# Kernel tuning notes

Hardware: AMD Instinct MI355X
Metric: run time of the kernel (lower is better)

The kernel has to match this reference:

```python
import jax, jax.numpy as jnp
import numpy as np
from jax import lax

STRIDE = 2
PADDING = 2
KERNEL = 5


def _conv_transpose3d(x, weight, bias):
    # weight: [C_in, C_out, kd, kh, kw] (PyTorch ConvTranspose3d layout)
    # Equivalent dense conv: flip kernel spatially, swap in/out channels,
    # lhs_dilation=stride, symmetric padding = dilation*(k-1) - padding.
    w_t = jnp.flip(weight, axis=(2, 3, 4)).transpose(1, 0, 2, 3, 4)  # [C_out, C_in, k,k,k]
    pad = KERNEL - 1 - PADDING  # = 2
    y = lax.conv_general_dilated(
        x, w_t,
        window_strides=(1, 1, 1),
        padding=[(pad, pad)] * 3,
        lhs_dilation=(STRIDE, STRIDE, STRIDE),
        dimension_numbers=("NCDHW", "OIDHW", "NCDHW"),
    )
    return y + bias[None, :, None, None, None]


def _maxpool3d(y, k):
    # PyTorch MaxPool3d(kernel=k) -> stride=k, no padding, floor mode == VALID
    win = (1, 1, k, k, k)
    return lax.reduce_window(y, -jnp.inf, lax.max, win, win, "VALID")


def setup_inputs() -> dict:
    key = jax.random.key(0)
    k1, k2, k3 = jax.random.split(key, 3)
    x = jax.random.normal(k1, (16, 32, 16, 32, 32), dtype=jnp.float32)
    weight = jax.random.normal(k2, (32, 64, 5, 5, 5), dtype=jnp.float32) * 0.05
    bias = jax.random.normal(k3, (64,), dtype=jnp.float32) * 0.05
    return {"x": x, "weight": weight, "bias": bias}


def reference(x, weight, bias):
    y = _conv_transpose3d(x, weight, bias)     # [16, 64, 31, 63, 63]
    y = _maxpool3d(y, 2)                       # [16, 64, 15, 31, 31]
    y = _maxpool3d(y, 3)                       # [16, 64, 5, 10, 10]
    return jnp.sum(y, axis=1, keepdims=True)   # [16, 1, 5, 10, 10]
```

## Files before the change

### kernel.cpp

```cpp
#include <hip/hip_runtime.h>
#include <hip/hip_bf16.h>
#include <math.h>

typedef short bf16x8 __attribute__((ext_vector_type(8)));
typedef float f32x4 __attribute__((ext_vector_type(4)));

constexpr int CIN = 32, COUT = 64, D = 16, H = 32, W = 32;

constexpr size_t WS_NEED = 884736u;

static __device__ const unsigned char IT_CODE[24] = {
    0, 8, 16, 3,
    1, 9, 17, 11, 19, 7,
    2, 10, 18, 5, 13, 21, 15,
    4, 12, 20, 6, 14, 22, 23};
static __device__ const unsigned char IT_START[5] = {0, 4, 10, 17, 24};
static __device__ const unsigned char EPI_START[10] = {0, 1, 3, 5, 6, 7, 9, 11, 12, 13};
static __device__ const unsigned char EPI_CNT[10]   = {1, 2, 2, 1, 1, 2, 2, 1, 1, 2};

__global__ void prep_w(const float* __restrict__ w, unsigned short* __restrict__ wtp) {
    int idx = blockIdx.x * 256 + threadIdx.x;
    int ci  = idx & 31;
    int co  = (idx >> 5) & 63;
    int tt  = idx >> 11;
    int t   = tt % 27, cls = tt / 27;
    int td = t / 9, th = (t / 3) % 3, tw = t % 3;
    int pd = (cls >> 2) & 1, ph = (cls >> 1) & 1, pw = cls & 1;
    int kd = pd + 2 * td, kh = ph + 2 * th, kw = pw + 2 * tw;
    float v = 0.f;
    if (kd < 5 && kh < 5 && kw < 5)
        v = w[(ci * COUT + co) * 125 + kd * 25 + kh * 5 + kw];
    __hip_bfloat16 b = __float2bfloat16(v);
    wtp[idx] = *reinterpret_cast<unsigned short*>(&b);
}

__device__ __forceinline__ int lpA(int wrow, int quad) {
    return wrow * 64 + ((quad ^ ((wrow >> 1) & 3)) << 4);
}

__global__ __launch_bounds__(256, 2) void main_k(
    const unsigned short* __restrict__ wtp, const float* __restrict__ x,
    const float* __restrict__ bias, float* __restrict__ out)
{
    __shared__ unsigned short Xs[25600];
    int bx = blockIdx.x;
    int h0 = bx % 10;
    int d0 = (bx / 10) % 5;
    int n  = bx / 50;
    int tid = threadIdx.x;

    int id0 = 3 * d0 - 1, ih0 = 3 * h0 - 1;
    for (int u = tid; u < 6400; u += 256) {
        int q  = u & 7;
        int ci = (u >> 3) & 31;
        int p  = u >> 8;
        int dd = p / 5, hl = p % 5;
        int id = id0 + dd, ih = ih0 + hl;
        float4 v = {0.f, 0.f, 0.f, 0.f};
        if (id >= 0 && ih >= 0)
            v = ((const float4*)(x + (((size_t)(n * CIN + ci) * D + id) * H + ih) * W))[q];
        unsigned short hj[4];
        {
            __hip_bfloat16 b0 = __float2bfloat16(v.x); hj[0] = *reinterpret_cast<unsigned short*>(&b0);
            __hip_bfloat16 b1 = __float2bfloat16(v.y); hj[1] = *reinterpret_cast<unsigned short*>(&b1);
            __hip_bfloat16 b2 = __float2bfloat16(v.z); hj[2] = *reinterpret_cast<unsigned short*>(&b2);
            __hip_bfloat16 b3 = __float2bfloat16(v.w); hj[3] = *reinterpret_cast<unsigned short*>(&b3);
        }
        int rowb = p * 1024;
        int cig = ci >> 3, cil = ci & 7;
#pragma unroll
        for (int j = 0; j < 4; ++j) {
            int ww = 4 * q + 1 + j;
            if (ww < 32)
                Xs[rowb + ww * 32 + ((cig ^ ((ww >> 1) & 3)) << 3) + cil] = hj[j];
        }
        if (q == 0)
            Xs[rowb + (cig << 3) + cil] = 0;
    }

    int lane = tid & 63, wv = tid >> 6;
    int l15 = lane & 15, quad = lane >> 4;
    int wv_s = __builtin_amdgcn_readfirstlane(wv);

    int laneB = l15 * 64 + quad * 16;
    int m1 = 16 + l15; if (m1 > 29) m1 = 29;
    int lp00 = lpA(l15 + 0, quad), lp01 = lpA(l15 + 1, quad), lp02 = lpA(l15 + 2, quad);
    int lp10 = lpA(m1 + 0, quad),  lp11 = lpA(m1 + 1, quad),  lp12 = lpA(m1 + 2, quad);

    f32x4 mx[2][4];
#pragma unroll
    for (int mt = 0; mt < 2; ++mt)
#pragma unroll
        for (int nt = 0; nt < 4; ++nt) mx[mt][nt] = (f32x4){-INFINITY, -INFINITY, -INFINITY, -INFINITY};

    __syncthreads();
    const char* xsb = (const char*)Xs;

    int it0 = IT_START[wv_s], it1 = IT_START[wv_s + 1];
#pragma unroll 1
    for (int ii = it0; ii < it1; ++ii) {
        int code  = __builtin_amdgcn_readfirstlane(IT_CODE[ii]);
        int cls   = code & 7;
        int alpha = code >> 3;
        int ntd = 3 - ((cls >> 2) & 1), nth = 3 - ((cls >> 1) & 1), ntw = 3 - (cls & 1);
        const char* tbb = (const char*)wtp + (size_t)cls * 27 * 4096 + laneB;
        const int T = ntd * nth * ntw;

        f32x4 acc[3][2][4];
#pragma unroll
        for (int b = 0; b < 3; ++b)
#pragma unroll
            for (int mt = 0; mt < 2; ++mt)
#pragma unroll
                for (int nt = 0; nt < 4; ++nt) acc[b][mt][nt] = (f32x4){0.f, 0.f, 0.f, 0.f};

        int ptd = 0, pth = 0, ptw = 0;
        auto adv = [&]() {
            ++ptw;
            if (ptw == ntw) { ptw = 0; ++pth; if (pth == nth) { pth = 0; ++ptd; } }
        };

        int Qb_e = ((alpha + 2) * 5 + 2) * 2048, ss_e = 2;
        bf16x8 bE0 = *(const bf16x8*)(tbb);
        bf16x8 bE1 = *(const bf16x8*)(tbb + 1024);
        bf16x8 bE2 = *(const bf16x8*)(tbb + 2048);
        bf16x8 bE3 = *(const bf16x8*)(tbb + 3072);
        adv();
        int Qb_o = ((alpha + 2 - ptd) * 5 + (2 - pth)) * 2048, ss_o = 2 - ptw;
        const char* bqo = tbb + (ptd * 9 + pth * 3 + ptw) * 4096;
        bf16x8 bO0 = *(const bf16x8*)(bqo);
        bf16x8 bO1 = *(const bf16x8*)(bqo + 1024);
        bf16x8 bO2 = *(const bf16x8*)(bqo + 2048);
        bf16x8 bO3 = *(const bf16x8*)(bqo + 3072);
        adv();

#pragma unroll 1
        for (int it = 0; it < T; it += 2) {
            {
                int lpa = ss_e == 0 ? lp00 : (ss_e == 1 ? lp01 : lp02);
                int lpb = ss_e == 0 ? lp10 : (ss_e == 1 ? lp11 : lp12);
#pragma unroll
                for (int beta = 0; beta < 3; ++beta) {
                    const char* rb = xsb + Qb_e + beta * 2048;
                    bf16x8 af0 = *(const bf16x8*)(rb + lpa);
                    bf16x8 af1 = *(const bf16x8*)(rb + lpb);
                    acc[beta][0][0] = __builtin_amdgcn_mfma_f32_16x16x32_bf16(af0, bE0, acc[beta][0][0], 0, 0, 0);
                    acc[beta][0][1] = __builtin_amdgcn_mfma_f32_16x16x32_bf16(af0, bE1, acc[beta][0][1], 0, 0, 0);
                    acc[beta][0][2] = __builtin_amdgcn_mfma_f32_16x16x32_bf16(af0, bE2, acc[beta][0][2], 0, 0, 0);
                    acc[beta][0][3] = __builtin_amdgcn_mfma_f32_16x16x32_bf16(af0, bE3, acc[beta][0][3], 0, 0, 0);
                    acc[beta][1][0] = __builtin_amdgcn_mfma_f32_16x16x32_bf16(af1, bE0, acc[beta][1][0], 0, 0, 0);
                    acc[beta][1][1] = __builtin_amdgcn_mfma_f32_16x16x32_bf16(af1, bE1, acc[beta][1][1], 0, 0, 0);
                    acc[beta][1][2] = __builtin_amdgcn_mfma_f32_16x16x32_bf16(af1, bE2, acc[beta][1][2], 0, 0, 0);
                    acc[beta][1][3] = __builtin_amdgcn_mfma_f32_16x16x32_bf16(af1, bE3, acc[beta][1][3], 0, 0, 0);
                }
            }
            if (it + 2 < T) {
                const char* bq = tbb + (ptd * 9 + pth * 3 + ptw) * 4096;
                Qb_e = ((alpha + 2 - ptd) * 5 + (2 - pth)) * 2048;
                ss_e = 2 - ptw;
                bE0 = *(const bf16x8*)(bq);
                bE1 = *(const bf16x8*)(bq + 1024);
                bE2 = *(const bf16x8*)(bq + 2048);
                bE3 = *(const bf16x8*)(bq + 3072);
                adv();
            }
            if (it + 1 < T) {
                {
                    int lpa = ss_o == 0 ? lp00 : (ss_o == 1 ? lp01 : lp02);
                    int lpb = ss_o == 0 ? lp10 : (ss_o == 1 ? lp11 : lp12);
#pragma unroll
                    for (int beta = 0; beta < 3; ++beta) {
                        const char* rb = xsb + Qb_o + beta * 2048;
                        bf16x8 af0 = *(const bf16x8*)(rb + lpa);
                        bf16x8 af1 = *(const bf16x8*)(rb + lpb);
                        acc[beta][0][0] = __builtin_amdgcn_mfma_f32_16x16x32_bf16(af0, bO0, acc[beta][0][0], 0, 0, 0);
                        acc[beta][0][1] = __builtin_amdgcn_mfma_f32_16x16x32_bf16(af0, bO1, acc[beta][0][1], 0, 0, 0);
                        acc[beta][0][2] = __builtin_amdgcn_mfma_f32_16x16x32_bf16(af0, bO2, acc[beta][0][2], 0, 0, 0);
                        acc[beta][0][3] = __builtin_amdgcn_mfma_f32_16x16x32_bf16(af0, bO3, acc[beta][0][3], 0, 0, 0);
                        acc[beta][1][0] = __builtin_amdgcn_mfma_f32_16x16x32_bf16(af1, bO0, acc[beta][1][0], 0, 0, 0);
                        acc[beta][1][1] = __builtin_amdgcn_mfma_f32_16x16x32_bf16(af1, bO1, acc[beta][1][1], 0, 0, 0);
                        acc[beta][1][2] = __builtin_amdgcn_mfma_f32_16x16x32_bf16(af1, bO2, acc[beta][1][2], 0, 0, 0);
                        acc[beta][1][3] = __builtin_amdgcn_mfma_f32_16x16x32_bf16(af1, bO3, acc[beta][1][3], 0, 0, 0);
                    }
                }
                if (it + 3 < T) {
                    const char* bq = tbb + (ptd * 9 + pth * 3 + ptw) * 4096;
                    Qb_o = ((alpha + 2 - ptd) * 5 + (2 - pth)) * 2048;
                    ss_o = 2 - ptw;
                    bO0 = *(const bf16x8*)(bq);
                    bO1 = *(const bf16x8*)(bq + 1024);
                    bO2 = *(const bf16x8*)(bq + 2048);
                    bO3 = *(const bf16x8*)(bq + 3072);
                    adv();
                }
            }
        }

#pragma unroll
        for (int mt = 0; mt < 2; ++mt)
#pragma unroll
            for (int nt = 0; nt < 4; ++nt)
#pragma unroll
                for (int r = 0; r < 4; ++r) {
                    float m = fmaxf(fmaxf(acc[0][mt][nt][r], acc[1][mt][nt][r]), acc[2][mt][nt][r]);
                    mx[mt][nt][r] = fmaxf(mx[mt][nt][r], m);
                }
    }

    __syncthreads();
    float* epi = (float*)Xs;
    int fsm0 = (0x3123 >> (quad * 4)) & 15;
    int fsm1 = (0x4312 >> (quad * 4)) & 15;
#pragma unroll
    for (int mt = 0; mt < 2; ++mt) {
        int fs = mt ? fsm1 : fsm0;
        int g  = mt * 4 + quad;
#pragma unroll
        for (int nt = 0; nt < 4; ++nt) {
            float a0 = mx[mt][nt][0], a1 = mx[mt][nt][1], a2 = mx[mt][nt][2], a3 = mx[mt][nt][3];
            float t01 = fmaxf(a0, a1), t012 = fmaxf(t01, a2), t0123 = fmaxf(t012, a3);
            float pA = fs == 1 ? a0 : (fs == 2 ? t01 : (fs == 3 ? t012 : t0123));
            float t23 = fmaxf(a2, a3), t123 = fmaxf(a1, t23);
            float pB = fs == 1 ? t123 : (fs == 2 ? t23 : (fs == 3 ? a3 : -INFINITY));
            epi[((wv * 8 + g) * 2 + 0) * 64 + nt * 16 + l15] = pA;
            epi[((wv * 8 + g) * 2 + 1) * 64 + nt * 16 + l15] = pB;
        }
    }
    __syncthreads();

    int elemBase = ((n * 5 + d0) * 10 + h0) * 10;
    float bco = bias[lane];
#pragma unroll 1
    for (int win = wv_s; win < 10; win += 4) {
        int st = EPI_START[win], cnt = EPI_CNT[win];
        float v = -INFINITY;
        for (int src = 0; src < 4; ++src)
            for (int e = st; e < st + cnt; ++e)
                v = fmaxf(v, epi[(src * 16 + e) * 64 + lane]);
        v += bco;
#pragma unroll
        for (int off = 32; off > 0; off >>= 1) v += __shfl_xor(v, off);
        if (lane == 0) out[elemBase + win] = v;
    }
}

__global__ __launch_bounds__(256) void fused_fallback(
    const float* __restrict__ x, const float* __restrict__ wsrc,
    const float* __restrict__ bias, float* __restrict__ out)
{
    __shared__ float xs[CIN * 125];
    __shared__ float wmax[4][64];
    const int b  = blockIdx.x;
    const int w0 = b % 10, h0 = (b / 10) % 10, d0 = (b / 100) % 5, n = b / 500;
    const int tid = threadIdx.x;
    const int id0 = 3 * d0 - 1, ih0 = 3 * h0 - 1, iw0 = 3 * w0 - 1;
    for (int e = tid; e < CIN * 125; e += 256) {
        int kk = e % 5, jj = (e / 5) % 5, ii = (e / 25) % 5, c = e / 125;
        int id = id0 + ii, ih = ih0 + jj, iw = iw0 + kk;
        float v = 0.f;
        if (id >= 0 && ih >= 0 && iw >= 0)
            v = x[(((n * CIN + c) * D + id) * H + ih) * W + iw];
        xs[e] = v;
    }
    __syncthreads();
    const int lane = tid & 63, wv = tid >> 6;
    float lmax = -INFINITY;
    for (int ccls = 0; ccls < 2; ++ccls) {
        const int cls = wv * 2 + ccls;
        const int pd = (cls >> 2) & 1, ph = (cls >> 1) & 1, pw = cls & 1;
        float acc[27];
#pragma unroll
        for (int i = 0; i < 27; ++i) acc[i] = 0.f;
        for (int ci = 0; ci < CIN; ++ci) {
            float wr[27];
#pragma unroll
            for (int t = 0; t < 27; ++t) {
                int td = t / 9, th = (t / 3) % 3, tw = t % 3;
                int kd = pd + 2 * td, kh = ph + 2 * th, kw = pw + 2 * tw;
                wr[t] = (kd < 5 && kh < 5 && kw < 5)
                          ? wsrc[((ci * 64 + lane) * 125) + kd * 25 + kh * 5 + kw] : 0.f;
            }
            const float* xb = xs + ci * 125;
#pragma unroll
            for (int td = 0; td < 3; ++td)
#pragma unroll
            for (int th = 0; th < 3; ++th)
#pragma unroll
            for (int tw = 0; tw < 3; ++tw) {
                const float wval = wr[(td * 3 + th) * 3 + tw];
#pragma unroll
                for (int a = 0; a < 3; ++a)
#pragma unroll
                for (int bb = 0; bb < 3; ++bb)
#pragma unroll
                for (int cc = 0; cc < 3; ++cc)
                    acc[(a * 3 + bb) * 3 + cc] +=
                        xb[(a + 2 - td) * 25 + (bb + 2 - th) * 5 + (cc + 2 - tw)] * wval;
            }
        }
#pragma unroll
        for (int i = 0; i < 27; ++i) lmax = fmaxf(lmax, acc[i]);
    }
    wmax[wv][lane] = lmax;
    __syncthreads();
    if (wv == 0) {
        float m = fmaxf(fmaxf(wmax[0][lane], wmax[1][lane]),
                        fmaxf(wmax[2][lane], wmax[3][lane]));
        m += bias[lane];
        for (int off = 32; off > 0; off >>= 1) m += __shfl_down(m, off);
        if (lane == 0) out[b] = m;
    }
}

extern "C" void kernel_launch(void* const* d_in, const int* in_sizes, int n_in,
                              void* d_out, int out_size, void* d_ws, size_t ws_size,
                              hipStream_t stream) {
    const float* x    = (const float*)d_in[0];
    const float* w    = (const float*)d_in[1];
    const float* bias = (const float*)d_in[2];
    float* out = (float*)d_out;

    if (ws_size >= WS_NEED) {
        unsigned short* wtp = (unsigned short*)d_ws;
        prep_w<<<1728, 256, 0, stream>>>(w, wtp);
        main_k<<<800, 256, 0, stream>>>(wtp, x, bias, out);
    } else {
        fused_fallback<<<8000, 256, 0, stream>>>(x, w, bias, out);
    }
}
```

Measured before the change: 206.1 us.

## Switch conv MFMA tiles to 32x32x16 and prefetch A fragments into registers

The main loop moves from 16x16x32 bf16 MFMA tiles to 32x32x16 tiles. Each wave now holds two 32-wide output-channel accumulators per beta instead of eight 16x16 ones, and the LDS A-operand addressing and swizzle are reworked to match. A fragments for the next tap are loaded into registers ahead of use, alongside the B fragments. The max-pool epilogue is remapped to the 32x32 accumulator layout. prep_w now reads the weights coalesced and writes only the taps that are actually used. The aim is fewer MFMA issues and fewer fragment loads per FLOP, plus hiding LDS latency. The cost is higher register pressure from the prefetched A fragments, which could hurt occupancy at 2 waves per SIMD.

```diff
diff --git a/kernel.cpp b/kernel.cpp
--- a/kernel.cpp
+++ b/kernel.cpp
@@ -3,7 +3,7 @@
 #include <math.h>
 
 typedef short bf16x8 __attribute__((ext_vector_type(8)));
-typedef float f32x4 __attribute__((ext_vector_type(4)));
+typedef float f32x16 __attribute__((ext_vector_type(16)));
 
 constexpr int CIN = 32, COUT = 64, D = 16, H = 32, W = 32;
 
@@ -15,27 +15,21 @@
     2, 10, 18, 5, 13, 21, 15,
     4, 12, 20, 6, 14, 22, 23};
 static __device__ const unsigned char IT_START[5] = {0, 4, 10, 17, 24};
-static __device__ const unsigned char EPI_START[10] = {0, 1, 3, 5, 6, 7, 9, 11, 12, 13};
-static __device__ const unsigned char EPI_CNT[10]   = {1, 2, 2, 1, 1, 2, 2, 1, 1, 2};
 
 __global__ void prep_w(const float* __restrict__ w, unsigned short* __restrict__ wtp) {
-    int idx = blockIdx.x * 256 + threadIdx.x;
-    int ci  = idx & 31;
-    int co  = (idx >> 5) & 63;
-    int tt  = idx >> 11;
-    int t   = tt % 27, cls = tt / 27;
-    int td = t / 9, th = (t / 3) % 3, tw = t % 3;
-    int pd = (cls >> 2) & 1, ph = (cls >> 1) & 1, pw = cls & 1;
-    int kd = pd + 2 * td, kh = ph + 2 * th, kw = pw + 2 * tw;
-    float v = 0.f;
-    if (kd < 5 && kh < 5 && kw < 5)
-        v = w[(ci * COUT + co) * 125 + kd * 25 + kh * 5 + kw];
+    int pair = blockIdx.x;
+    int k = threadIdx.x;
+    if (k >= 125) return;
+    int ci = pair >> 6, co = pair & 63;
+    float v = w[(size_t)pair * 125 + k];
+    int kd = k / 25, kh = (k / 5) % 5, kw = k % 5;
+    int pd = kd & 1, td = kd >> 1;
+    int ph = kh & 1, th = kh >> 1;
+    int pw = kw & 1, tw = kw >> 1;
+    int cls = pd * 4 + ph * 2 + pw;
+    int t   = td * 9 + th * 3 + tw;
     __hip_bfloat16 b = __float2bfloat16(v);
-    wtp[idx] = *reinterpret_cast<unsigned short*>(&b);
-}
-
-__device__ __forceinline__ int lpA(int wrow, int quad) {
-    return wrow * 64 + ((quad ^ ((wrow >> 1) & 3)) << 4);
+    wtp[((cls * 27 + t) * 64 + co) * 32 + ci] = *reinterpret_cast<unsigned short*>(&b);
 }
 
 __global__ __launch_bounds__(256, 2) void main_k(
@@ -79,19 +73,25 @@
     }
 
     int lane = tid & 63, wv = tid >> 6;
-    int l15 = lane & 15, quad = lane >> 4;
+    int l31 = lane & 31, hh2 = lane >> 5;
     int wv_s = __builtin_amdgcn_readfirstlane(wv);
 
-    int laneB = l15 * 64 + quad * 16;
-    int m1 = 16 + l15; if (m1 > 29) m1 = 29;
-    int lp00 = lpA(l15 + 0, quad), lp01 = lpA(l15 + 1, quad), lp02 = lpA(l15 + 2, quad);
-    int lp10 = lpA(m1 + 0, quad),  lp11 = lpA(m1 + 1, quad),  lp12 = lpA(m1 + 2, quad);
-
-    f32x4 mx[2][4];
-#pragma unroll
-    for (int mt = 0; mt < 2; ++mt)
-#pragma unroll
-        for (int nt = 0; nt < 4; ++nt) mx[mt][nt] = (f32x4){-INFINITY, -INFINITY, -INFINITY, -INFINITY};
+    int laneB = l31 * 64 + hh2 * 16;
+    int m_c = l31 > 29 ? 29 : l31;
+    int lp[3][2];
+#pragma unroll
+    for (int s = 0; s < 3; ++s)
+#pragma unroll
+        for (int f = 0; f < 2; ++f) {
+            int R = m_c + s;
+            lp[s][f] = R * 64 + (((2 * f + hh2) ^ ((R >> 1) & 3)) << 4);
+        }
+
+    f32x16 mx[2];
+#pragma unroll
+    for (int nh = 0; nh < 2; ++nh)
+#pragma unroll
+        for (int r = 0; r < 16; ++r) mx[nh][r] = -INFINITY;
 
     __syncthreads();
     const char* xsb = (const char*)Xs;
@@ -106,13 +106,13 @@
         const char* tbb = (const char*)wtp + (size_t)cls * 27 * 4096 + laneB;
         const int T = ntd * nth * ntw;
 
-        f32x4 acc[3][2][4];
+        f32x16 acc[3][2];
 #pragma unroll
         for (int b = 0; b < 3; ++b)
 #pragma unroll
-            for (int mt = 0; mt < 2; ++mt)
-#pragma unroll
-                for (int nt = 0; nt < 4; ++nt) acc[b][mt][nt] = (f32x4){0.f, 0.f, 0.f, 0.f};
+            for (int nh = 0; nh < 2; ++nh)
+#pragma unroll
+                for (int r = 0; r < 16; ++r) acc[b][nh][r] = 0.f;
 
         int ptd = 0, pth = 0, ptw = 0;
         auto adv = [&]() {
@@ -120,111 +120,138 @@
             if (ptw == ntw) { ptw = 0; ++pth; if (pth == nth) { pth = 0; ++ptd; } }
         };
 
-        int Qb_e = ((alpha + 2) * 5 + 2) * 2048, ss_e = 2;
-        bf16x8 bE0 = *(const bf16x8*)(tbb);
-        bf16x8 bE1 = *(const bf16x8*)(tbb + 1024);
-        bf16x8 bE2 = *(const bf16x8*)(tbb + 2048);
-        bf16x8 bE3 = *(const bf16x8*)(tbb + 3072);
+        bf16x8 bE00, bE01, bE10, bE11, aE[3][2];
+        {
+            bE00 = *(const bf16x8*)(tbb);
+            bE01 = *(const bf16x8*)(tbb + 32);
+            bE10 = *(const bf16x8*)(tbb + 2048);
+            bE11 = *(const bf16x8*)(tbb + 2080);
+            const char* rb = xsb + ((alpha + 2) * 5 + 2) * 2048;
+#pragma unroll
+            for (int b = 0; b < 3; ++b) {
+                aE[b][0] = *(const bf16x8*)(rb + b * 2048 + lp[2][0]);
+                aE[b][1] = *(const bf16x8*)(rb + b * 2048 + lp[2][1]);
+            }
+        }
         adv();
-        int Qb_o = ((alpha + 2 - ptd) * 5 + (2 - pth)) * 2048, ss_o = 2 - ptw;
-        const char* bqo = tbb + (ptd * 9 + pth * 3 + ptw) * 4096;
-        bf16x8 bO0 = *(const bf16x8*)(bqo);
-        bf16x8 bO1 = *(const bf16x8*)(bqo + 1024);
-        bf16x8 bO2 = *(const bf16x8*)(bqo + 2048);
-        bf16x8 bO3 = *(const bf16x8*)(bqo + 3072);
+        bf16x8 bO00, bO01, bO10, bO11, aO[3][2];
+        {
+            const char* bq = tbb + (ptd * 9 + pth * 3 + ptw) * 4096;
+            bO00 = *(const bf16x8*)(bq);
+            bO01 = *(const bf16x8*)(bq + 32);
+            bO10 = *(const bf16x8*)(bq + 2048);
+            bO11 = *(const bf16x8*)(bq + 2080);
+            int ss = 2 - ptw;
+            int lpa0 = ss == 0 ? lp[0][0] : (ss == 1 ? lp[1][0] : lp[2][0]);
+            int lpa1 = ss == 0 ? lp[0][1] : (ss == 1 ? lp[1][1] : lp[2][1]);
+            const char* rb = xsb + ((alpha + 2 - ptd) * 5 + (2 - pth)) * 2048;
+#pragma unroll
+            for (int b = 0; b < 3; ++b) {
+                aO[b][0] = *(const bf16x8*)(rb + b * 2048 + lpa0);
+                aO[b][1] = *(const bf16x8*)(rb + b * 2048 + lpa1);
+            }
+        }
         adv();
 
 #pragma unroll 1
         for (int it = 0; it < T; it += 2) {
-            {
-                int lpa = ss_e == 0 ? lp00 : (ss_e == 1 ? lp01 : lp02);
-                int lpb = ss_e == 0 ? lp10 : (ss_e == 1 ? lp11 : lp12);
-#pragma unroll
-                for (int beta = 0; beta < 3; ++beta) {
-                    const char* rb = xsb + Qb_e + beta * 2048;
-                    bf16x8 af0 = *(const bf16x8*)(rb + lpa);
-                    bf16x8 af1 = *(const bf16x8*)(rb + lpb);
-                    acc[beta][0][0] = __builtin_amdgcn_mfma_f32_16x16x32_bf16(af0, bE0, acc[beta][0][0], 0, 0, 0);
-                    acc[beta][0][1] = __builtin_amdgcn_mfma_f32_16x16x32_bf16(af0, bE1, acc[beta][0][1], 0, 0, 0);
-                    acc[beta][0][2] = __builtin_amdgcn_mfma_f32_16x16x32_bf16(af0, bE2, acc[beta][0][2], 0, 0, 0);
-                    acc[beta][0][3] = __builtin_amdgcn_mfma_f32_16x16x32_bf16(af0, bE3, acc[beta][0][3], 0, 0, 0);
-                    acc[beta][1][0] = __builtin_amdgcn_mfma_f32_16x16x32_bf16(af1, bE0, acc[beta][1][0], 0, 0, 0);
-                    acc[beta][1][1] = __builtin_amdgcn_mfma_f32_16x16x32_bf16(af1, bE1, acc[beta][1][1], 0, 0, 0);
-                    acc[beta][1][2] = __builtin_amdgcn_mfma_f32_16x16x32_bf16(af1, bE2, acc[beta][1][2], 0, 0, 0);
-                    acc[beta][1][3] = __builtin_amdgcn_mfma_f32_16x16x32_bf16(af1, bE3, acc[beta][1][3], 0, 0, 0);
-                }
+#pragma unroll
+            for (int b = 0; b < 3; ++b) {
+                acc[b][0] = __builtin_amdgcn_mfma_f32_32x32x16_bf16(aE[b][0], bE00, acc[b][0], 0, 0, 0);
+                acc[b][1] = __builtin_amdgcn_mfma_f32_32x32x16_bf16(aE[b][0], bE10, acc[b][1], 0, 0, 0);
+            }
+#pragma unroll
+            for (int b = 0; b < 3; ++b) {
+                acc[b][0] = __builtin_amdgcn_mfma_f32_32x32x16_bf16(aE[b][1], bE01, acc[b][0], 0, 0, 0);
+                acc[b][1] = __builtin_amdgcn_mfma_f32_32x32x16_bf16(aE[b][1], bE11, acc[b][1], 0, 0, 0);
             }
             if (it + 2 < T) {
                 const char* bq = tbb + (ptd * 9 + pth * 3 + ptw) * 4096;
-                Qb_e = ((alpha + 2 - ptd) * 5 + (2 - pth)) * 2048;
-                ss_e = 2 - ptw;
-                bE0 = *(const bf16x8*)(bq);
-                bE1 = *(const bf16x8*)(bq + 1024);
-                bE2 = *(const bf16x8*)(bq + 2048);
-                bE3 = *(const bf16x8*)(bq + 3072);
+                bE00 = *(const bf16x8*)(bq);
+                bE01 = *(const bf16x8*)(bq + 32);
+                bE10 = *(const bf16x8*)(bq + 2048);
+                bE11 = *(const bf16x8*)(bq + 2080);
+                int ss = 2 - ptw;
+                int lpa0 = ss == 0 ? lp[0][0] : (ss == 1 ? lp[1][0] : lp[2][0]);
+                int lpa1 = ss == 0 ? lp[0][1] : (ss == 1 ? lp[1][1] : lp[2][1]);
+                const char* rb = xsb + ((alpha + 2 - ptd) * 5 + (2 - pth)) * 2048;
+#pragma unroll
+                for (int b = 0; b < 3; ++b) {
+                    aE[b][0] = *(const bf16x8*)(rb + b * 2048 + lpa0);
+                    aE[b][1] = *(const bf16x8*)(rb + b * 2048 + lpa1);
+                }
                 adv();
             }
             if (it + 1 < T) {
-                {
-                    int lpa = ss_o == 0 ? lp00 : (ss_o == 1 ? lp01 : lp02);
-                    int lpb = ss_o == 0 ? lp10 : (ss_o == 1 ? lp11 : lp12);
-#pragma unroll
-                    for (int beta = 0; beta < 3; ++beta) {
-                        const char* rb = xsb + Qb_o + beta * 2048;
-                        bf16x8 af0 = *(const bf16x8*)(rb + lpa);
-                        bf16x8 af1 = *(const bf16x8*)(rb + lpb);
-                        acc[beta][0][0] = __builtin_amdgcn_mfma_f32_16x16x32_bf16(af0, bO0, acc[beta][0][0], 0, 0, 0);
-                        acc[beta][0][1] = __builtin_amdgcn_mfma_f32_16x16x32_bf16(af0, bO1, acc[beta][0][1], 0, 0, 0);
-                        acc[beta][0][2] = __builtin_amdgcn_mfma_f32_16x16x32_bf16(af0, bO2, acc[beta][0][2], 0, 0, 0);
-                        acc[beta][0][3] = __builtin_amdgcn_mfma_f32_16x16x32_bf16(af0, bO3, acc[beta][0][3], 0, 0, 0);
-                        acc[beta][1][0] = __builtin_amdgcn_mfma_f32_16x16x32_bf16(af1, bO0, acc[beta][1][0], 0, 0, 0);
-                        acc[beta][1][1] = __builtin_amdgcn_mfma_f32_16x16x32_bf16(af1, bO1, acc[beta][1][1], 0, 0, 0);
-                        acc[beta][1][2] = __builtin_amdgcn_mfma_f32_16x16x32_bf16(af1, bO2, acc[beta][1][2], 0, 0, 0);
-                        acc[beta][1][3] = __builtin_amdgcn_mfma_f32_16x16x32_bf16(af1, bO3, acc[beta][1][3], 0, 0, 0);
-                    }
+#pragma unroll
+                for (int b = 0; b < 3; ++b) {
+                    acc[b][0] = __builtin_amdgcn_mfma_f32_32x32x16_bf16(aO[b][0], bO00, acc[b][0], 0, 0, 0);
+                    acc[b][1] = __builtin_amdgcn_mfma_f32_32x32x16_bf16(aO[b][0], bO10, acc[b][1], 0, 0, 0);
+                }
+#pragma unroll
+                for (int b = 0; b < 3; ++b) {
+                    acc[b][0] = __builtin_amdgcn_mfma_f32_32x32x16_bf16(aO[b][1], bO01, acc[b][0], 0, 0, 0);
+                    acc[b][1] = __builtin_amdgcn_mfma_f32_32x32x16_bf16(aO[b][1], bO11, acc[b][1], 0, 0, 0);
                 }
                 if (it + 3 < T) {
                     const char* bq = tbb + (ptd * 9 + pth * 3 + ptw) * 4096;
-                    Qb_o = ((alpha + 2 - ptd) * 5 + (2 - pth)) * 2048;
-                    ss_o = 2 - ptw;
-                    bO0 = *(const bf16x8*)(bq);
-                    bO1 = *(const bf16x8*)(bq + 1024);
-                    bO2 = *(const bf16x8*)(bq + 2048);
-                    bO3 = *(const bf16x8*)(bq + 3072);
+                    bO00 = *(const bf16x8*)(bq);
+                    bO01 = *(const bf16x8*)(bq + 32);
+                    bO10 = *(const bf16x8*)(bq + 2048);
+                    bO11 = *(const bf16x8*)(bq + 2080);
+                    int ss = 2 - ptw;
+                    int lpa0 = ss == 0 ? lp[0][0] : (ss == 1 ? lp[1][0] : lp[2][0]);
+                    int lpa1 = ss == 0 ? lp[0][1] : (ss == 1 ? lp[1][1] : lp[2][1]);
+                    const char* rb = xsb + ((alpha + 2 - ptd) * 5 + (2 - pth)) * 2048;
+#pragma unroll
+                    for (int b = 0; b < 3; ++b) {
+                        aO[b][0] = *(const bf16x8*)(rb + b * 2048 + lpa0);
+                        aO[b][1] = *(const bf16x8*)(rb + b * 2048 + lpa1);
+                    }
                     adv();
                 }
             }
         }
 
 #pragma unroll
-        for (int mt = 0; mt < 2; ++mt)
-#pragma unroll
-            for (int nt = 0; nt < 4; ++nt)
-#pragma unroll
-                for (int r = 0; r < 4; ++r) {
-                    float m = fmaxf(fmaxf(acc[0][mt][nt][r], acc[1][mt][nt][r]), acc[2][mt][nt][r]);
-                    mx[mt][nt][r] = fmaxf(mx[mt][nt][r], m);
-                }
+        for (int nh = 0; nh < 2; ++nh)
+#pragma unroll
+            for (int r = 0; r < 16; ++r) {
+                float m = fmaxf(fmaxf(acc[0][nh][r], acc[1][nh][r]), acc[2][nh][r]);
+                mx[nh][r] = fmaxf(mx[nh][r], m);
+            }
     }
 
     __syncthreads();
     float* epi = (float*)Xs;
-    int fsm0 = (0x3123 >> (quad * 4)) & 15;
-    int fsm1 = (0x4312 >> (quad * 4)) & 15;
-#pragma unroll
-    for (int mt = 0; mt < 2; ++mt) {
-        int fs = mt ? fsm1 : fsm0;
-        int g  = mt * 4 + quad;
-#pragma unroll
-        for (int nt = 0; nt < 4; ++nt) {
-            float a0 = mx[mt][nt][0], a1 = mx[mt][nt][1], a2 = mx[mt][nt][2], a3 = mx[mt][nt][3];
-            float t01 = fmaxf(a0, a1), t012 = fmaxf(t01, a2), t0123 = fmaxf(t012, a3);
-            float pA = fs == 1 ? a0 : (fs == 2 ? t01 : (fs == 3 ? t012 : t0123));
-            float t23 = fmaxf(a2, a3), t123 = fmaxf(a1, t23);
-            float pB = fs == 1 ? t123 : (fs == 2 ? t23 : (fs == 3 ? a3 : -INFINITY));
-            epi[((wv * 8 + g) * 2 + 0) * 64 + nt * 16 + l15] = pA;
-            epi[((wv * 8 + g) * 2 + 1) * 64 + nt * 16 + l15] = pB;
-        }
+#pragma unroll
+    for (int nh = 0; nh < 2; ++nh) {
+        float wp[10];
+#pragma unroll
+        for (int i = 0; i < 10; ++i) wp[i] = -INFINITY;
+        const f32x16& v = mx[nh];
+        if (hh2 == 0) {
+            wp[0] = fmaxf(fmaxf(v[0], v[1]), v[2]);
+            wp[1] = v[3];
+            wp[2] = v[4];
+            wp[3] = fmaxf(fmaxf(v[5], v[6]), v[7]);
+            wp[5] = fmaxf(v[8], v[9]);
+            wp[6] = fmaxf(v[10], v[11]);
+            wp[8] = fmaxf(fmaxf(v[12], v[13]), v[14]);
+            wp[9] = v[15];
+        } else {
+            wp[1] = fmaxf(v[0], v[1]);
+            wp[2] = fmaxf(v[2], v[3]);
+            wp[4] = fmaxf(fmaxf(v[4], v[5]), v[6]);
+            wp[5] = v[7];
+            wp[6] = v[8];
+            wp[7] = fmaxf(fmaxf(v[9], v[10]), v[11]);
+            wp[9] = fmaxf(v[12], v[13]);
+        }
+        int col = nh * 32 + l31;
+#pragma unroll
+        for (int win = 0; win < 10; ++win)
+            epi[((wv * 2 + hh2) * 10 + win) * 64 + col] = wp[win];
     }
     __syncthreads();
 
@@ -232,11 +259,10 @@
     float bco = bias[lane];
 #pragma unroll 1
     for (int win = wv_s; win < 10; win += 4) {
-        int st = EPI_START[win], cnt = EPI_CNT[win];
         float v = -INFINITY;
-        for (int src = 0; src < 4; ++src)
-            for (int e = st; e < st + cnt; ++e)
-                v = fmaxf(v, epi[(src * 16 + e) * 64 + lane]);
+#pragma unroll
+        for (int src = 0; src < 8; ++src)
+            v = fmaxf(v, epi[(src * 10 + win) * 64 + lane]);
         v += bco;
 #pragma unroll
         for (int off = 32; off > 0; off >>= 1) v += __shfl_xor(v, off);
@@ -322,7 +348,7 @@
 
     if (ws_size >= WS_NEED) {
         unsigned short* wtp = (unsigned short*)d_ws;
-        prep_w<<<1728, 256, 0, stream>>>(w, wtp);
+        prep_w<<<2048, 128, 0, stream>>>(w, wtp);
         main_k<<<800, 256, 0, stream>>>(wtp, x, bias, out);
     } else {
         fused_fallback<<<8000, 256, 0, stream>>>(x, w, bias, out);
```

After: 214.6 us. 4.1% more time.
